# Kernel optimization log

Hardware: AMD Instinct MI355X
Metric: run time of the kernel (lower is better)

## Reference

```python
import jax, jax.numpy as jnp
import numpy as np

B = 2048
D = 40960          # util.half_kp_numel(): 64 king squares * 640 piece-square planes
BASE = 288
MOVE = 4096        # util.move_numel(): 64 from-squares * 64 to-squares
MOVE_SIZE = (64, 64)


def setup_inputs() -> dict:
    key = jax.random.key(0)
    ks = jax.random.split(key, 24)
    f32 = jnp.float32
    # forward args: sparse one-hot half-kp occupancy vectors (modeled as rand floats)
    pov = (jax.random.uniform(ks[0], (B, 1), f32) > 0.5).astype(f32)
    white = (jax.random.uniform(ks[1], (B, D), f32) < 0.001).astype(f32)
    black = (jax.random.uniform(ks[2], (B, D), f32) < 0.001).astype(f32)
    s = 0.01
    p = {
        'W_w': jax.random.normal(ks[3], (BASE, D), f32) * s,
        'b_w': jnp.zeros((BASE,), f32),
        'W_b': jax.random.normal(ks[4], (BASE, D), f32) * s,
        'b_b': jnp.zeros((BASE,), f32),
        'W_v0': jax.random.normal(ks[5], (32, 2 * BASE), f32) * s,
        'b_v0': jnp.zeros((32,), f32),
        'W_v1': jax.random.normal(ks[6], (32, 32), f32) * s,
        'b_v1': jnp.zeros((32,), f32),
        'W_v2': jax.random.normal(ks[7], (1, 32), f32) * s,
        'b_v2': jnp.zeros((1,), f32),
        'W_a0': jax.random.normal(ks[8], (144, 2 * BASE), f32) * s,
        'b_a0': jnp.zeros((144,), f32),
        'W_a1': jax.random.normal(ks[9], (MOVE, 144), f32) * s,
        'b_a1': jnp.zeros((MOVE,), f32),
        'W_vs': jax.random.normal(ks[10], (1, 2 * BASE), f32) * s,
        'b_vs': jnp.zeros((1,), f32),
        'W_as': jax.random.normal(ks[11], (MOVE, 2 * BASE), f32) * s,
        'b_as': jnp.zeros((MOVE,), f32),
    }
    return dict(pov=pov, white=white, black=black, **p)


def _linear(x, W, b):
    return x @ W.T + b


def reference(pov, white, black, W_w, b_w, W_b, b_b,
              W_v0, b_v0, W_v1, b_v1, W_v2, b_v2,
              W_a0, b_a0, W_a1, b_a1, W_vs, b_vs, W_as, b_as):
    # half-kp affine accumulators (the sparse gather-sum candidate)
    w256 = _linear(white, W_w, b_w)            # [B, BASE]
    b256 = _linear(black, W_b, b_b)            # [B, BASE]
    cat_wb = jnp.concatenate([w256, b256], axis=1)
    cat_bw = jnp.concatenate([b256, w256], axis=1)
    base = jax.nn.relu(pov * cat_wb + (1.0 - pov) * cat_bw)  # [B, 2*BASE]
    # value head with skip
    val = jax.nn.relu(_linear(base, W_v0, b_v0))
    val = jax.nn.relu(_linear(val, W_v1, b_v1))
    val = _linear(val, W_v2, b_v2) + _linear(base, W_vs, b_vs)   # [B, 1]
    # action head with skip
    act = jax.nn.relu(_linear(base, W_a0, b_a0))
    act = _linear(act, W_a1, b_a1) + _linear(base, W_as, b_as)   # [B, MOVE]
    act = act.reshape(act.shape[0], *MOVE_SIZE)                  # [B, 64, 64]
    return (val, act)
```

## Files before the change

kernel.cpp:

```cpp
#include <hip/hip_runtime.h>

#define D_IN 40960
#define NB 2048
#define BASEN 288
#define CAPL 95
#define KP 736

typedef __attribute__((ext_vector_type(4))) float f32x4;
typedef __attribute__((ext_vector_type(8))) short short8;

__device__ inline float bf2f(ushort u) {
    unsigned v = ((unsigned)u) << 16; float f; __builtin_memcpy(&f, &v, 4); return f;
}
__device__ inline ushort f2bf(float f) {
    unsigned x; __builtin_memcpy(&x, &f, 4);
    unsigned r = (x + 0x7FFFu + ((x >> 16) & 1u)) >> 16; return (ushort)r;
}

__device__ inline void llds16(const void* g, void* l) {
    __builtin_amdgcn_global_load_lds((const __attribute__((address_space(1))) unsigned*)g,
                                     (__attribute__((address_space(3))) unsigned*)l, 16, 0, 0);
}

__global__ __launch_bounds__(256) void transpose_kernel(const float* __restrict__ Ww,
                                                        const float* __restrict__ Wb,
                                                        ushort* __restrict__ Wtw,
                                                        ushort* __restrict__ Wtb) {
    const float* src = blockIdx.z ? Wb : Ww;
    ushort* dst = blockIdx.z ? Wtb : Wtw;
    __shared__ float tile[32][65];
    int i = threadIdx.x;
    int d0 = blockIdx.x * 64, o0 = blockIdx.y * 32;
    int tr = i >> 4, tc4 = (i & 15) * 4;
#pragma unroll
    for (int rep = 0; rep < 2; ++rep) {
        int row = tr + rep * 16;
        float4 u = *(const float4*)&src[(size_t)(o0 + row) * D_IN + d0 + tc4];
        tile[row][tc4] = u.x; tile[row][tc4 + 1] = u.y; tile[row][tc4 + 2] = u.z; tile[row][tc4 + 3] = u.w;
    }
    __syncthreads();
    int dr = i >> 3, oc4 = (i & 7) * 4;
#pragma unroll
    for (int rep = 0; rep < 2; ++rep) {
        int d = dr + rep * 32;
        ushort4 u;
        u.x = f2bf(tile[oc4][d]); u.y = f2bf(tile[oc4 + 1][d]);
        u.z = f2bf(tile[oc4 + 2][d]); u.w = f2bf(tile[oc4 + 3][d]);
        *(ushort4*)&dst[(size_t)(d0 + d) * BASEN + o0 + oc4] = u;
    }
}

__global__ __launch_bounds__(256) void prep_kernel(const float* __restrict__ W_a1,
                                                   const float* __restrict__ W_as,
                                                   const float* __restrict__ b_a1,
                                                   const float* __restrict__ b_as,
                                                   const float* __restrict__ W_a0,
                                                   const float* __restrict__ W_v0,
                                                   ushort* __restrict__ Wcat,
                                                   float* __restrict__ biasA,
                                                   ushort* __restrict__ Wa0h,
                                                   ushort* __restrict__ Wv0h) {
    int m = blockIdx.x, t = threadIdx.x;
    if (m < 4096) {
        ushort* dst = Wcat + (size_t)m * KP;
        if (t < 144) dst[t] = f2bf(W_a1[(size_t)m * 144 + t]);
        if (t >= 144 && t < 160) dst[t] = 0;
        for (int j = t; j < 576; j += 256) dst[160 + j] = f2bf(W_as[(size_t)m * 576 + j]);
        if (t == 200) biasA[m] = b_a1[m] + b_as[m];
    } else if (m < 4096 + 144) {
        int r = m - 4096;
        for (int j = t; j < 576; j += 256) Wa0h[(size_t)r * 576 + j] = f2bf(W_a0[(size_t)r * 576 + j]);
    } else {
        int r = m - (4096 + 144);
        for (int j = t; j < 576; j += 256) Wv0h[(size_t)r * 576 + j] = f2bf(W_v0[(size_t)r * 576 + j]);
    }
}

__global__ __launch_bounds__(320) void scan_kernel(const float* __restrict__ white,
                                                   const float* __restrict__ black,
                                                   const ushort* __restrict__ Wtw,
                                                   const ushort* __restrict__ Wtb,
                                                   const float* __restrict__ b_w,
                                                   const float* __restrict__ b_b,
                                                   float* __restrict__ accG) {
    const int row = blockIdx.x;
    const int colr = blockIdx.y;
    const int t = threadIdx.x;
    __shared__ int cnt;
    __shared__ int idx[CAPL];
    if (t == 0) cnt = 0;
    __syncthreads();

    const uint4* src = (const uint4*)((colr ? black : white) + (size_t)row * D_IN);
    const int NV = D_IN / 4;
#pragma unroll
    for (int base = 0; base < NV; base += 320 * 8) {
        uint4 x[8];
#pragma unroll
        for (int u = 0; u < 8; ++u) x[u] = src[base + u * 320 + t];
#pragma unroll
        for (int u = 0; u < 8; ++u) {
            uint4 v = x[u];
            if (v.x | v.y | v.z | v.w) {
                int i4 = (base + u * 320 + t) * 4;
                if (v.x) { int p = atomicAdd(&cnt, 1); if (p < CAPL) idx[p] = i4; }
                if (v.y) { int p = atomicAdd(&cnt, 1); if (p < CAPL) idx[p] = i4 + 1; }
                if (v.z) { int p = atomicAdd(&cnt, 1); if (p < CAPL) idx[p] = i4 + 2; }
                if (v.w) { int p = atomicAdd(&cnt, 1); if (p < CAPL) idx[p] = i4 + 3; }
            }
        }
    }
    __syncthreads();

    if (t < BASEN) {
        const ushort* Wt = colr ? Wtb : Wtw;
        int n = min(cnt, CAPL);
        float acc = colr ? b_b[t] : b_w[t];
#pragma unroll 4
        for (int i = 0; i < n; ++i) acc += bf2f(Wt[(size_t)idx[i] * BASEN + t]);
        accG[((size_t)colr * NB + row) * BASEN + t] = acc;
    }
}

__global__ __launch_bounds__(576) void head_kernel(const float* __restrict__ accG,
                                                   const float* __restrict__ pov,
                                                   const ushort* __restrict__ Wa0h,
                                                   const float* __restrict__ b_a0,
                                                   const ushort* __restrict__ Wv0h,
                                                   const float* __restrict__ b_v0,
                                                   const float* __restrict__ W_v1,
                                                   const float* __restrict__ b_v1,
                                                   const float* __restrict__ W_v2,
                                                   const float* __restrict__ b_v2,
                                                   const float* __restrict__ W_vs,
                                                   const float* __restrict__ b_vs,
                                                   ushort* __restrict__ hidden,
                                                   float* __restrict__ outv) {
    int b = blockIdx.x, t = threadIdx.x;
    __shared__ float baseS[576];
    __shared__ float v0s[32];
    __shared__ float skipS;

    float p = pov[b];
    ushort* hrow = hidden + (size_t)b * KP;
    if (t < BASEN) {
        float aW = accG[(size_t)b * BASEN + t];
        float aB = accG[(size_t)NB * BASEN + (size_t)b * BASEN + t];
        float b0 = fmaxf(p * aW + (1.0f - p) * aB, 0.0f);
        float b1 = fmaxf(p * aB + (1.0f - p) * aW, 0.0f);
        baseS[t] = b0; baseS[BASEN + t] = b1;
        hrow[160 + t] = f2bf(b0);
        hrow[160 + BASEN + t] = f2bf(b1);
        if (t < 16) hrow[144 + t] = 0;
    }
    __syncthreads();

    {
        int o = t >> 2, q4 = t & 3;
        const ushort* wr = Wa0h + (size_t)o * 576 + q4 * 144;
        const float* bp = &baseS[q4 * 144];
        float s = 0.f;
#pragma unroll
        for (int j = 0; j < 144; j += 8) {
            uint4 q = *(const uint4*)(wr + j);
            s += bp[j + 0] * bf2f((ushort)(q.x & 0xFFFF)) + bp[j + 1] * bf2f((ushort)(q.x >> 16))
               + bp[j + 2] * bf2f((ushort)(q.y & 0xFFFF)) + bp[j + 3] * bf2f((ushort)(q.y >> 16))
               + bp[j + 4] * bf2f((ushort)(q.z & 0xFFFF)) + bp[j + 5] * bf2f((ushort)(q.z >> 16))
               + bp[j + 6] * bf2f((ushort)(q.w & 0xFFFF)) + bp[j + 7] * bf2f((ushort)(q.w >> 16));
        }
        s += __shfl_xor(s, 1);
        s += __shfl_xor(s, 2);
        if (q4 == 0) hrow[o] = f2bf(fmaxf(s + b_a0[o], 0.f));
    }

    if (t < 512) {
        int o = t >> 4, sub = t & 15;
        const ushort* wr = Wv0h + (size_t)o * 576 + sub * 36;
        const float* bp = &baseS[sub * 36];
        float s = 0.f;
#pragma unroll
        for (int j = 0; j < 36; j += 4) {
            ushort4 q = *(const ushort4*)(wr + j);
            s += bp[j + 0] * bf2f(q.x) + bp[j + 1] * bf2f(q.y)
               + bp[j + 2] * bf2f(q.z) + bp[j + 3] * bf2f(q.w);
        }
        s += __shfl_xor(s, 1); s += __shfl_xor(s, 2);
        s += __shfl_xor(s, 4); s += __shfl_xor(s, 8);
        if (sub == 0) v0s[o] = fmaxf(s + b_v0[o], 0.f);
    } else {
        int u = t - 512;
        const float* wp = W_vs + u * 9;
        const float* bp = &baseS[u * 9];
        float s = 0.f;
#pragma unroll
        for (int j = 0; j < 9; ++j) s += bp[j] * wp[j];
        s += __shfl_xor(s, 1); s += __shfl_xor(s, 2); s += __shfl_xor(s, 4);
        s += __shfl_xor(s, 8); s += __shfl_xor(s, 16); s += __shfl_xor(s, 32);
        if (u == 0) skipS = s;
    }
    __syncthreads();

    if (t < 32) {
        float s = b_v1[t];
        const float* w = W_v1 + (size_t)t * 32;
#pragma unroll
        for (int j = 0; j < 32; ++j) s += v0s[j] * w[j];
        float part = fmaxf(s, 0.f) * W_v2[t];
        part += __shfl_xor(part, 1); part += __shfl_xor(part, 2); part += __shfl_xor(part, 4);
        part += __shfl_xor(part, 8); part += __shfl_xor(part, 16);
        if (t == 0) outv[b] = part + b_v2[0] + skipS + b_vs[0];
    }
}

__global__ __launch_bounds__(256) void gemm_act(const ushort* __restrict__ A,
                                                const ushort* __restrict__ Bm,
                                                const float* __restrict__ biasA,
                                                float* __restrict__ outa) {
    __shared__ ushort As[128 * 32];
    __shared__ ushort Bs[128 * 32];
    int tid = threadIdx.x;
    int lane = tid & 63, wv = tid >> 6;
    int bm = blockIdx.x, bn = blockIdx.y;
    int wm = wv & 1, wn = wv >> 1;
    f32x4 acc[4][4];
#pragma unroll
    for (int mt = 0; mt < 4; ++mt)
#pragma unroll
        for (int nt = 0; nt < 4; ++nt) { f32x4 z = {0.f, 0.f, 0.f, 0.f}; acc[mt][nt] = z; }

    int r = tid >> 2, c8 = (tid & 3) * 8;
    const ushort* Ag = A  + (size_t)(bm * 128 + r) * KP + c8;
    const ushort* Bg = Bm + (size_t)(bn * 128 + r) * KP + c8;
    ushort* AsW = As + wv * 512;
    ushort* BsW = Bs + wv * 512;

    int kg = (lane >> 4) * 8;
    int rA = wm * 64 + (lane & 15);
    int rB = wn * 64 + (lane & 15);

    for (int kk = 0; kk < KP; kk += 32) {
        llds16(Ag + kk, AsW);
        llds16(Ag + (size_t)64 * KP + kk, AsW + 2048);
        llds16(Bg + kk, BsW);
        llds16(Bg + (size_t)64 * KP + kk, BsW + 2048);
        __syncthreads();
        short8 af[4], bf[4];
#pragma unroll
        for (int mt = 0; mt < 4; ++mt) af[mt] = *(const short8*)&As[(rA + mt * 16) * 32 + kg];
#pragma unroll
        for (int nt = 0; nt < 4; ++nt) bf[nt] = *(const short8*)&Bs[(rB + nt * 16) * 32 + kg];
#pragma unroll
        for (int mt = 0; mt < 4; ++mt)
#pragma unroll
            for (int nt = 0; nt < 4; ++nt)
                acc[mt][nt] = __builtin_amdgcn_mfma_f32_16x16x32_bf16(af[mt], bf[nt], acc[mt][nt], 0, 0, 0);
        __syncthreads();
    }

    int colb = bn * 128 + wn * 64 + (lane & 15);
    int rowb = bm * 128 + wm * 64 + ((lane >> 4) << 2);
#pragma unroll
    for (int nt = 0; nt < 4; ++nt) {
        float bia = biasA[colb + nt * 16];
#pragma unroll
        for (int mt = 0; mt < 4; ++mt) {
#pragma unroll
            for (int q = 0; q < 4; ++q) {
                int rr = rowb + mt * 16 + q;
                outa[(size_t)rr * 4096 + colb + nt * 16] = acc[mt][nt][q] + bia;
            }
        }
    }
}

extern "C" void kernel_launch(void* const* d_in, const int* in_sizes, int n_in,
                              void* d_out, int out_size, void* d_ws, size_t ws_size,
                              hipStream_t stream) {
    const float* pov   = (const float*)d_in[0];
    const float* white = (const float*)d_in[1];
    const float* black = (const float*)d_in[2];
    const float* W_w   = (const float*)d_in[3];
    const float* b_w   = (const float*)d_in[4];
    const float* W_b   = (const float*)d_in[5];
    const float* b_b   = (const float*)d_in[6];
    const float* W_v0  = (const float*)d_in[7];
    const float* b_v0  = (const float*)d_in[8];
    const float* W_v1  = (const float*)d_in[9];
    const float* b_v1  = (const float*)d_in[10];
    const float* W_v2  = (const float*)d_in[11];
    const float* b_v2  = (const float*)d_in[12];
    const float* W_a0  = (const float*)d_in[13];
    const float* b_a0  = (const float*)d_in[14];
    const float* W_a1  = (const float*)d_in[15];
    const float* b_a1  = (const float*)d_in[16];
    const float* W_vs  = (const float*)d_in[17];
    const float* b_vs  = (const float*)d_in[18];
    const float* W_as  = (const float*)d_in[19];
    const float* b_as  = (const float*)d_in[20];

    char* ws = (char*)d_ws;
    ushort* Wtw   = (ushort*)(ws + 0);
    ushort* Wtb   = (ushort*)(ws + 23592960);
    ushort* hidden= (ushort*)(ws + 47185920);
    ushort* Wcat  = (ushort*)(ws + 50200576);
    float*  biasA = (float*)(ws + 56229888);
    ushort* Wa0h  = (ushort*)(ws + 56246272);
    ushort* Wv0h  = (ushort*)(ws + 56412160);
    float*  accG  = (float*)(ws + 56449024);

    float* outp = (float*)d_out;

    transpose_kernel<<<dim3(D_IN / 64, BASEN / 32, 2), 256, 0, stream>>>(W_w, W_b, Wtw, Wtb);
    prep_kernel<<<4096 + 144 + 32, 256, 0, stream>>>(W_a1, W_as, b_a1, b_as, W_a0, W_v0,
                                                     Wcat, biasA, Wa0h, Wv0h);
    scan_kernel<<<dim3(NB, 2), 320, 0, stream>>>(white, black, Wtw, Wtb, b_w, b_b, accG);
    head_kernel<<<NB, 576, 0, stream>>>(accG, pov, Wa0h, b_a0, Wv0h, b_v0,
                                        W_v1, b_v1, W_v2, b_v2, W_vs, b_vs, hidden, outp);
    gemm_act<<<dim3(2048 / 128, 4096 / 128), 256, 0, stream>>>(hidden, Wcat, biasA, outp + 2048);
}
```

Baseline: 846.0 us.

## Widen weight transpose writes and restructure sparse scan loads and gathers

```diff
diff --git a/kernel.cpp b/kernel.cpp
--- a/kernel.cpp
+++ b/kernel.cpp
@@ -26,27 +26,33 @@
                                                         const float* __restrict__ Wb,
                                                         ushort* __restrict__ Wtw,
                                                         ushort* __restrict__ Wtb) {
-    const float* src = blockIdx.z ? Wb : Ww;
-    ushort* dst = blockIdx.z ? Wtb : Wtw;
-    __shared__ float tile[32][65];
-    int i = threadIdx.x;
-    int d0 = blockIdx.x * 64, o0 = blockIdx.y * 32;
-    int tr = i >> 4, tc4 = (i & 15) * 4;
-#pragma unroll
-    for (int rep = 0; rep < 2; ++rep) {
-        int row = tr + rep * 16;
-        float4 u = *(const float4*)&src[(size_t)(o0 + row) * D_IN + d0 + tc4];
-        tile[row][tc4] = u.x; tile[row][tc4 + 1] = u.y; tile[row][tc4 + 2] = u.z; tile[row][tc4 + 3] = u.w;
-    }
-    __syncthreads();
-    int dr = i >> 3, oc4 = (i & 7) * 4;
-#pragma unroll
-    for (int rep = 0; rep < 2; ++rep) {
-        int d = dr + rep * 32;
-        ushort4 u;
-        u.x = f2bf(tile[oc4][d]); u.y = f2bf(tile[oc4 + 1][d]);
-        u.z = f2bf(tile[oc4 + 2][d]); u.w = f2bf(tile[oc4 + 3][d]);
-        *(ushort4*)&dst[(size_t)(d0 + d) * BASEN + o0 + oc4] = u;
+    const float* src = blockIdx.y ? Wb : Ww;
+    ushort* dst = blockIdx.y ? Wtb : Wtw;
+    __shared__ float lt[32][292];
+    int t = threadIdx.x;
+    int d0 = blockIdx.x * 32;
+    int orr = t >> 3, dc = (t & 7) * 4;
+#pragma unroll
+    for (int p = 0; p < 9; ++p) {
+        int o = p * 32 + orr;
+        float4 u = *(const float4*)&src[(size_t)o * D_IN + d0 + dc];
+        lt[dc][o] = u.x; lt[dc + 1][o] = u.y; lt[dc + 2][o] = u.z; lt[dc + 3][o] = u.w;
+    }
+    __syncthreads();
+    ushort* db = dst + (size_t)d0 * BASEN;
+#pragma unroll
+    for (int p = 0; p < 5; ++p) {
+        int s = p * 256 + t;
+        if (s < 1152) {
+            int d = s / 36, m = s - d * 36;
+            const float* lp = &lt[d][m * 8];
+            short8 v;
+            v[0] = (short)f2bf(lp[0]); v[1] = (short)f2bf(lp[1]);
+            v[2] = (short)f2bf(lp[2]); v[3] = (short)f2bf(lp[3]);
+            v[4] = (short)f2bf(lp[4]); v[5] = (short)f2bf(lp[5]);
+            v[6] = (short)f2bf(lp[6]); v[7] = (short)f2bf(lp[7]);
+            *(short8*)&db[s * 8] = v;
+        }
     }
 }
 
@@ -76,7 +82,7 @@
     }
 }
 
-__global__ __launch_bounds__(320) void scan_kernel(const float* __restrict__ white,
+__global__ __launch_bounds__(256) void scan_kernel(const float* __restrict__ white,
                                                    const float* __restrict__ black,
                                                    const ushort* __restrict__ Wtw,
                                                    const ushort* __restrict__ Wtb,
@@ -92,17 +98,16 @@
     __syncthreads();
 
     const uint4* src = (const uint4*)((colr ? black : white) + (size_t)row * D_IN);
-    const int NV = D_IN / 4;
-#pragma unroll
-    for (int base = 0; base < NV; base += 320 * 8) {
-        uint4 x[8];
-#pragma unroll
-        for (int u = 0; u < 8; ++u) x[u] = src[base + u * 320 + t];
-#pragma unroll
-        for (int u = 0; u < 8; ++u) {
+#pragma unroll
+    for (int b16 = 0; b16 < 2; ++b16) {
+        uint4 x[16];
+#pragma unroll
+        for (int u = 0; u < 16; ++u) x[u] = src[b16 * 4096 + u * 256 + t];
+#pragma unroll
+        for (int u = 0; u < 16; ++u) {
             uint4 v = x[u];
             if (v.x | v.y | v.z | v.w) {
-                int i4 = (base + u * 320 + t) * 4;
+                int i4 = (b16 * 4096 + u * 256 + t) * 4;
                 if (v.x) { int p = atomicAdd(&cnt, 1); if (p < CAPL) idx[p] = i4; }
                 if (v.y) { int p = atomicAdd(&cnt, 1); if (p < CAPL) idx[p] = i4 + 1; }
                 if (v.z) { int p = atomicAdd(&cnt, 1); if (p < CAPL) idx[p] = i4 + 2; }
@@ -110,15 +115,37 @@
             }
         }
     }
-    __syncthreads();
-
-    if (t < BASEN) {
+    {
+        uint4 x[8];
+#pragma unroll
+        for (int u = 0; u < 8; ++u) x[u] = src[8192 + u * 256 + t];
+#pragma unroll
+        for (int u = 0; u < 8; ++u) {
+            uint4 v = x[u];
+            if (v.x | v.y | v.z | v.w) {
+                int i4 = (8192 + u * 256 + t) * 4;
+                if (v.x) { int p = atomicAdd(&cnt, 1); if (p < CAPL) idx[p] = i4; }
+                if (v.y) { int p = atomicAdd(&cnt, 1); if (p < CAPL) idx[p] = i4 + 1; }
+                if (v.z) { int p = atomicAdd(&cnt, 1); if (p < CAPL) idx[p] = i4 + 2; }
+                if (v.w) { int p = atomicAdd(&cnt, 1); if (p < CAPL) idx[p] = i4 + 3; }
+            }
+        }
+    }
+    __syncthreads();
+
+    if (t < 144) {
         const ushort* Wt = colr ? Wtb : Wtw;
+        const float* bb = colr ? b_b : b_w;
         int n = min(cnt, CAPL);
-        float acc = colr ? b_b[t] : b_w[t];
+        float a0 = bb[2 * t], a1 = bb[2 * t + 1];
 #pragma unroll 4
-        for (int i = 0; i < n; ++i) acc += bf2f(Wt[(size_t)idx[i] * BASEN + t]);
-        accG[((size_t)colr * NB + row) * BASEN + t] = acc;
+        for (int i = 0; i < n; ++i) {
+            unsigned q = *(const unsigned*)&Wt[(size_t)idx[i] * BASEN + 2 * t];
+            a0 += bf2f((ushort)(q & 0xFFFF));
+            a1 += bf2f((ushort)(q >> 16));
+        }
+        float2 r; r.x = a0; r.y = a1;
+        *(float2*)&accG[((size_t)colr * NB + row) * BASEN + 2 * t] = r;
     }
 }
 
@@ -310,10 +337,10 @@
 
     float* outp = (float*)d_out;
 
-    transpose_kernel<<<dim3(D_IN / 64, BASEN / 32, 2), 256, 0, stream>>>(W_w, W_b, Wtw, Wtb);
+    transpose_kernel<<<dim3(D_IN / 32, 2), 256, 0, stream>>>(W_w, W_b, Wtw, Wtb);
     prep_kernel<<<4096 + 144 + 32, 256, 0, stream>>>(W_a1, W_as, b_a1, b_as, W_a0, W_v0,
                                                      Wcat, biasA, Wa0h, Wv0h);
-    scan_kernel<<<dim3(NB, 2), 320, 0, stream>>>(white, black, Wtw, Wtb, b_w, b_b, accG);
+    scan_kernel<<<dim3(NB, 2), 256, 0, stream>>>(white, black, Wtw, Wtb, b_w, b_b, accG);
     head_kernel<<<NB, 576, 0, stream>>>(accG, pov, Wa0h, b_a0, Wv0h, b_v0,
                                         W_v1, b_v1, W_v2, b_v2, W_vs, b_vs, hidden, outp);
     gemm_act<<<dim3(2048 / 128, 4096 / 128), 256, 0, stream>>>(hidden, Wcat, biasA, outp + 2048);
```

Measured after the change: 841.0 us. Within noise of the previous version (-0.6%).
